# Performance work log

Measured on AMD Instinct MI355X. Metric: run time of the kernel, lower is better.

The kernel has to match this reference:

```python
import jax, jax.numpy as jnp
import numpy as np

B, C, H, W = 2048, 256, 7, 7
EPS = 1e-6  # torch.nn.CosineSimilarity eps


def _masked_cos_loss(f1, f2, A):
    """Fused all-pairs masked cosine similarity.
    f1, f2: [B, C, H, W]; A: [H, W, H, W] binary mask.
    Replaces the original 7x7x7x7 Python loop of per-pixel CosineSimilarity calls.
    Returns per-batch loss [B]: sum_{ijkl: A==1} cos(f1[:,:,i,j], f2[:,:,k,l]) / (H*W*H*W).
    """
    n1 = jnp.linalg.norm(f1, axis=1)  # [B, H, W]
    n2 = jnp.linalg.norm(f2, axis=1)  # [B, H, W]
    dot = jnp.einsum('bcij,bckl->bijkl', f1, f2)  # [B, H, W, H, W]
    denom = jnp.maximum(n1[:, :, :, None, None] * n2[:, None, None, :, :], EPS)
    cos = dot / denom
    mask = (A == 1).astype(f1.dtype)
    return jnp.einsum('bijkl,ijkl->b', cos, mask) / (H * W * H * W)


def setup_inputs() -> dict:
    key = jax.random.key(0)
    k1, k2, k3, k4 = jax.random.split(key, 4)
    base_feature = jax.random.normal(k1, (B, C, H, W), dtype=jnp.float32)
    moment_feature = jax.random.normal(k2, (B, C, H, W), dtype=jnp.float32)
    base_A = jax.random.randint(k3, (H, W, H, W), 0, 2, dtype=jnp.int32)
    moment_A = jax.random.randint(k4, (H, W, H, W), 0, 2, dtype=jnp.int32)
    return {"base_feature": base_feature, "moment_feature": moment_feature,
            "base_A": base_A, "moment_A": moment_A}


def reference(base_feature, moment_feature, base_A, moment_A):
    # base_loss  = masked cos(base[i,j],   moment[k,l]) under base_A
    # moment_loss = masked cos(moment[i,j], base[k,l])  under moment_A
    base_loss = _masked_cos_loss(base_feature, moment_feature, base_A)
    moment_loss = _masked_cos_loss(moment_feature, base_feature, moment_A)
    return -base_loss - moment_loss  # [B]
```

## Files before the change

### kernel.cpp

```cpp
#include <hip/hip_runtime.h>
#include <math.h>


constexpr int NB     = 2048;
constexpr int NC     = 256;
constexpr int NP     = 49;
constexpr int SLAB_C = 16;
constexpr int SLAB_F = SLAB_C * NP;
constexpr int NSLAB  = NC / SLAB_C;
constexpr float EPS  = 1e-6f;

__global__ __launch_bounds__(256, 2)
void pixpro_kernel(const float* __restrict__ gbase,
                   const float* __restrict__ gmom,
                   const int*   __restrict__ A1,
                   const int*   __restrict__ A2,
                   float*       __restrict__ out)
{
    __shared__ float wt[NP * NP];
    __shared__ __align__(16) float slab[4][2 * SLAB_F];

    const int tid  = threadIdx.x;
    const int wave = tid >> 6;
    const int lane = tid & 63;
    const int b    = blockIdx.x * 4 + wave;

    for (int t = tid; t < NP * NP; t += 256) {
        int p = t / NP, q = t - p * NP;
        wt[t] = (A1[t] == 1 ? 1.0f : 0.0f) + (A2[q * NP + p] == 1 ? 1.0f : 0.0f);
    }
    __syncthreads();

    float* sl = slab[wave];

    const int lp = lane & 7, lq = lane >> 3;
    const int p0 = (lp < 7 ? lp : 6) * 7;
    const int q0 = (lq < 7 ? lq : 6) * 7;

    const float* gb = gbase + (size_t)b * (NC * NP);
    const float* gm = gmom  + (size_t)b * (NC * NP);

    const float* vA = sl + ((lane < NP) ? lane : (SLAB_F - NP + lane));
    const float* vB = sl + (SLAB_F + 15 + (lane < 34 ? lane : 33));
    const float* bp = sl + p0;
    const float* mp = sl + SLAB_F + q0;

    float acc[7][7];
    #pragma unroll
    for (int j = 0; j < 7; ++j)
        #pragma unroll
        for (int i = 0; i < 7; ++i) acc[j][i] = 0.0f;
    float nrm0 = 0.0f, nrm1 = 0.0f;

    float4 rb0 = {}, rb1 = {}, rb2 = {}, rb3 = {};
    float4 rm0 = {}, rm1 = {}, rm2 = {}, rm3 = {};
    {
        const float4* pb = (const float4*)gb;
        const float4* pm = (const float4*)gm;
        rb0 = pb[lane]; rb1 = pb[lane + 64]; rb2 = pb[lane + 128];
        rm0 = pm[lane]; rm1 = pm[lane + 64]; rm2 = pm[lane + 128];
        if (lane < 4) { rb3 = pb[lane + 192]; rm3 = pm[lane + 192]; }
    }

    for (int s = 0; s < NSLAB; ++s) {
        {
            float4* lb = (float4*)sl;
            float4* lm = (float4*)(sl + SLAB_F);
            lb[lane] = rb0; lb[lane + 64] = rb1; lb[lane + 128] = rb2;
            lm[lane] = rm0; lm[lane + 64] = rm1; lm[lane + 128] = rm2;
            if (lane < 4) { lb[lane + 192] = rb3; lm[lane + 192] = rm3; }
        }
        if (s + 1 < NSLAB) {
            const float4* pb = (const float4*)(gb + (s + 1) * SLAB_F);
            const float4* pm = (const float4*)(gm + (s + 1) * SLAB_F);
            rb0 = pb[lane]; rb1 = pb[lane + 64]; rb2 = pb[lane + 128];
            rm0 = pm[lane]; rm1 = pm[lane + 64]; rm2 = pm[lane + 128];
            if (lane < 4) { rb3 = pb[lane + 192]; rm3 = pm[lane + 192]; }
        }
        __syncthreads();

        #pragma unroll
        for (int c = 0; c < SLAB_C; ++c) {
            float bv[7], mv[7];
            #pragma unroll
            for (int i = 0; i < 7; ++i) bv[i] = bp[c * NP + i];
            #pragma unroll
            for (int j = 0; j < 7; ++j) mv[j] = mp[c * NP + j];
            float v0 = vA[c * NP];
            float v1 = vB[c * NP];
            nrm0 = fmaf(v0, v0, nrm0);
            nrm1 = fmaf(v1, v1, nrm1);
            #pragma unroll
            for (int j = 0; j < 7; ++j)
                #pragma unroll
                for (int i = 0; i < 7; ++i)
                    acc[j][i] = fmaf(bv[i], mv[j], acc[j][i]);
        }
        __syncthreads();
    }

    float* nsq = sl;
    nsq[lane] = nrm0;
    if (lane < 34) nsq[64 + lane] = nrm1;
    __syncthreads();

    float nbv[7], nmv[7];
    #pragma unroll
    for (int i = 0; i < 7; ++i) nbv[i] = sqrtf(nsq[p0 + i]);
    #pragma unroll
    for (int j = 0; j < 7; ++j) nmv[j] = sqrtf(nsq[NP + q0 + j]);

    float sum = 0.0f;
    if (lp < 7 && lq < 7) {
        #pragma unroll
        for (int j = 0; j < 7; ++j) {
            #pragma unroll
            for (int i = 0; i < 7; ++i) {
                float w     = wt[(p0 + i) * NP + (q0 + j)];
                float denom = fmaxf(nbv[i] * nmv[j], EPS);
                sum += w * acc[j][i] / denom;
            }
        }
    }

    #pragma unroll
    for (int m = 32; m; m >>= 1) sum += __shfl_xor(sum, m, 64);

    if (lane == 0) out[b] = sum * (-1.0f / 2401.0f);
}

extern "C" void kernel_launch(void* const* d_in, const int* in_sizes, int n_in,
                              void* d_out, int out_size, void* d_ws, size_t ws_size,
                              hipStream_t stream)
{
    (void)in_sizes; (void)n_in; (void)d_ws; (void)ws_size; (void)out_size;
    const float* base = (const float*)d_in[0];
    const float* mom  = (const float*)d_in[1];
    const int*   A1   = (const int*)d_in[2];
    const int*   A2   = (const int*)d_in[3];
    float*       out  = (float*)d_out;

    pixpro_kernel<<<NB / 4, 256, 0, stream>>>(base, mom, A1, A2, out);
}
```

Before: 243.5 us.

## Split channel reduction across two waves per batch with transposed LDS layout

Each batch is now handled by two waves, each reducing half of the channels, with partial dot products and norms combined through shared memory at the end. The LDS slab is transposed to a pixel-major layout with pitch 12 so the inner loop can use float4 reads along channels. Block-wide barriers in the main loop become per-wave lgkmcnt waits, the mask table is stored as bytes, and occupancy is raised to 4 blocks per SM. This doubles the number of waves to expose more parallelism and reduce LDS load instructions. The cost is an extra cross-wave reduction of 49 accumulators per thread and scattered scalar LDS stores.

```diff
diff --git a/kernel.cpp b/kernel.cpp
--- a/kernel.cpp
+++ b/kernel.cpp
@@ -5,45 +5,60 @@
 constexpr int NB     = 2048;
 constexpr int NC     = 256;
 constexpr int NP     = 49;
-constexpr int SLAB_C = 16;
-constexpr int SLAB_F = SLAB_C * NP;
-constexpr int NSLAB  = NC / SLAB_C;
+constexpr int SLAB_C = 8;
+constexpr int PITCH  = 12;
+constexpr int FWORDS = NP * PITCH;
+constexpr int REGION = 1280;
+constexpr int NSLABW = (NC / 2) / SLAB_C;
 constexpr float EPS  = 1e-6f;
 
-__global__ __launch_bounds__(256, 2)
+__global__ __launch_bounds__(256, 4)
 void pixpro_kernel(const float* __restrict__ gbase,
                    const float* __restrict__ gmom,
                    const int*   __restrict__ A1,
                    const int*   __restrict__ A2,
                    float*       __restrict__ out)
 {
-    __shared__ float wt[NP * NP];
-    __shared__ __align__(16) float slab[4][2 * SLAB_F];
+    __shared__ unsigned char wtb[NP * NP];
+    __shared__ __align__(16) float slab[4][REGION];
 
     const int tid  = threadIdx.x;
     const int wave = tid >> 6;
     const int lane = tid & 63;
-    const int b    = blockIdx.x * 4 + wave;
+    const int b    = blockIdx.x * 2 + (wave >> 1);
+    const int half = wave & 1;
 
     for (int t = tid; t < NP * NP; t += 256) {
         int p = t / NP, q = t - p * NP;
-        wt[t] = (A1[t] == 1 ? 1.0f : 0.0f) + (A2[q * NP + p] == 1 ? 1.0f : 0.0f);
+        wtb[t] = (unsigned char)((A1[t] == 1 ? 1 : 0) + (A2[q * NP + p] == 1 ? 1 : 0));
     }
     __syncthreads();
 
-    float* sl = slab[wave];
+    float* const sl  = slab[wave];
+    float* const slb = sl;
+    float* const slm = sl + FWORDS;
 
     const int lp = lane & 7, lq = lane >> 3;
     const int p0 = (lp < 7 ? lp : 6) * 7;
     const int q0 = (lq < 7 ? lq : 6) * 7;
 
-    const float* gb = gbase + (size_t)b * (NC * NP);
-    const float* gm = gmom  + (size_t)b * (NC * NP);
+    const float* gb = gbase + (size_t)b * (NC * NP) + (size_t)half * (128 * NP);
+    const float* gm = gmom  + (size_t)b * (NC * NP) + (size_t)half * (128 * NP);
 
-    const float* vA = sl + ((lane < NP) ? lane : (SLAB_F - NP + lane));
-    const float* vB = sl + (SLAB_F + 15 + (lane < 34 ? lane : 33));
-    const float* bp = sl + p0;
-    const float* mp = sl + SLAB_F + q0;
+    int wof[8];
+    #pragma unroll
+    for (int u = 0; u < 4; ++u) {
+        int e  = 4 * lane + u;
+        wof[u] = (e - 49 * (e / 49)) * PITCH + (e / 49);
+        int e2 = (lane < 34) ? (256 + 4 * lane + u) : 391;
+        wof[4 + u] = (e2 - 49 * (e2 / 49)) * PITCH + (e2 / 49);
+    }
+
+    const float* const vA = (lane < NP) ? (slb + lane * PITCH)
+                                        : (slm + (lane - NP) * PITCH);
+    const float* const vB = slm + ((lane < 34) ? (15 + lane) : 48) * PITCH;
+    const float* const bp = slb + p0 * PITCH;
+    const float* const mp = slm + q0 * PITCH;
 
     float acc[7][7];
     #pragma unroll
@@ -52,81 +67,110 @@
         for (int i = 0; i < 7; ++i) acc[j][i] = 0.0f;
     float nrm0 = 0.0f, nrm1 = 0.0f;
 
-    float4 rb0 = {}, rb1 = {}, rb2 = {}, rb3 = {};
-    float4 rm0 = {}, rm1 = {}, rm2 = {}, rm3 = {};
+    float4 rb0 = {}, rb1 = {}, rm0 = {}, rm1 = {};
     {
         const float4* pb = (const float4*)gb;
         const float4* pm = (const float4*)gm;
-        rb0 = pb[lane]; rb1 = pb[lane + 64]; rb2 = pb[lane + 128];
-        rm0 = pm[lane]; rm1 = pm[lane + 64]; rm2 = pm[lane + 128];
-        if (lane < 4) { rb3 = pb[lane + 192]; rm3 = pm[lane + 192]; }
+        rb0 = pb[lane]; rm0 = pm[lane];
+        if (lane < 34) { rb1 = pb[64 + lane]; rm1 = pm[64 + lane]; }
     }
 
-    for (int s = 0; s < NSLAB; ++s) {
-        {
-            float4* lb = (float4*)sl;
-            float4* lm = (float4*)(sl + SLAB_F);
-            lb[lane] = rb0; lb[lane + 64] = rb1; lb[lane + 128] = rb2;
-            lm[lane] = rm0; lm[lane + 64] = rm1; lm[lane + 128] = rm2;
-            if (lane < 4) { lb[lane + 192] = rb3; lm[lane + 192] = rm3; }
+    for (int s = 0; s < NSLABW; ++s) {
+        slb[wof[0]] = rb0.x; slb[wof[1]] = rb0.y; slb[wof[2]] = rb0.z; slb[wof[3]] = rb0.w;
+        slm[wof[0]] = rm0.x; slm[wof[1]] = rm0.y; slm[wof[2]] = rm0.z; slm[wof[3]] = rm0.w;
+        if (lane < 34) {
+            slb[wof[4]] = rb1.x; slb[wof[5]] = rb1.y; slb[wof[6]] = rb1.z; slb[wof[7]] = rb1.w;
+            slm[wof[4]] = rm1.x; slm[wof[5]] = rm1.y; slm[wof[6]] = rm1.z; slm[wof[7]] = rm1.w;
         }
-        if (s + 1 < NSLAB) {
-            const float4* pb = (const float4*)(gb + (s + 1) * SLAB_F);
-            const float4* pm = (const float4*)(gm + (s + 1) * SLAB_F);
-            rb0 = pb[lane]; rb1 = pb[lane + 64]; rb2 = pb[lane + 128];
-            rm0 = pm[lane]; rm1 = pm[lane + 64]; rm2 = pm[lane + 128];
-            if (lane < 4) { rb3 = pb[lane + 192]; rm3 = pm[lane + 192]; }
+        if (s + 1 < NSLABW) {
+            const float4* pb = (const float4*)(gb + (s + 1) * (SLAB_C * NP));
+            const float4* pm = (const float4*)(gm + (s + 1) * (SLAB_C * NP));
+            rb0 = pb[lane]; rm0 = pm[lane];
+            if (lane < 34) { rb1 = pb[64 + lane]; rm1 = pm[64 + lane]; }
         }
-        __syncthreads();
+        asm volatile("s_waitcnt lgkmcnt(0)" ::: "memory");
 
         #pragma unroll
-        for (int c = 0; c < SLAB_C; ++c) {
-            float bv[7], mv[7];
+        for (int c0 = 0; c0 < SLAB_C; c0 += 4) {
+            float4 mv[7];
             #pragma unroll
-            for (int i = 0; i < 7; ++i) bv[i] = bp[c * NP + i];
+            for (int j = 0; j < 7; ++j)
+                mv[j] = *(const float4*)(mp + j * PITCH + c0);
+            float4 a4 = *(const float4*)(vA + c0);
+            float4 b4 = *(const float4*)(vB + c0);
+            nrm0 = fmaf(a4.x, a4.x, fmaf(a4.y, a4.y, fmaf(a4.z, a4.z, fmaf(a4.w, a4.w, nrm0))));
+            nrm1 = fmaf(b4.x, b4.x, fmaf(b4.y, b4.y, fmaf(b4.z, b4.z, fmaf(b4.w, b4.w, nrm1))));
             #pragma unroll
-            for (int j = 0; j < 7; ++j) mv[j] = mp[c * NP + j];
-            float v0 = vA[c * NP];
-            float v1 = vB[c * NP];
-            nrm0 = fmaf(v0, v0, nrm0);
-            nrm1 = fmaf(v1, v1, nrm1);
+            for (int i = 0; i < 7; ++i) {
+                float4 bv = *(const float4*)(bp + i * PITCH + c0);
+                #pragma unroll
+                for (int j = 0; j < 7; ++j) {
+                    float t0 = fmaf(bv.x, mv[j].x, acc[j][i]);
+                    t0       = fmaf(bv.y, mv[j].y, t0);
+                    t0       = fmaf(bv.z, mv[j].z, t0);
+                    acc[j][i] = fmaf(bv.w, mv[j].w, t0);
+                }
+            }
+        }
+        asm volatile("s_waitcnt lgkmcnt(0)" ::: "memory");
+    }
+
+    __syncthreads();
+
+    float* const ex   = slab[wave & ~1];
+    const bool active = (lp < 7) && (lq < 7);
+    const int  tix    = lq * 7 + lp;
+
+    if (half) {
+        ex[lane]      = nrm0;
+        ex[64 + lane] = nrm1;
+        if (active) {
             #pragma unroll
             for (int j = 0; j < 7; ++j)
                 #pragma unroll
                 for (int i = 0; i < 7; ++i)
-                    acc[j][i] = fmaf(bv[i], mv[j], acc[j][i]);
+                    ex[128 + tix * 49 + j * 7 + i] = acc[j][i];
         }
-        __syncthreads();
     }
-
-    float* nsq = sl;
-    nsq[lane] = nrm0;
-    if (lane < 34) nsq[64 + lane] = nrm1;
     __syncthreads();
 
-    float nbv[7], nmv[7];
-    #pragma unroll
-    for (int i = 0; i < 7; ++i) nbv[i] = sqrtf(nsq[p0 + i]);
-    #pragma unroll
-    for (int j = 0; j < 7; ++j) nmv[j] = sqrtf(nsq[NP + q0 + j]);
+    if (!half) {
+        nrm0 += ex[lane];
+        nrm1 += ex[64 + lane];
+        if (active) {
+            #pragma unroll
+            for (int j = 0; j < 7; ++j)
+                #pragma unroll
+                for (int i = 0; i < 7; ++i)
+                    acc[j][i] += ex[128 + tix * 49 + j * 7 + i];
+        }
+        asm volatile("s_waitcnt lgkmcnt(0)" ::: "memory");
 
-    float sum = 0.0f;
-    if (lp < 7 && lq < 7) {
+        ex[lane] = nrm0;
+        if (lane < 34) ex[64 + lane] = nrm1;
+        asm volatile("s_waitcnt lgkmcnt(0)" ::: "memory");
+
+        float nbv[7], nmv[7];
         #pragma unroll
-        for (int j = 0; j < 7; ++j) {
+        for (int i = 0; i < 7; ++i) nbv[i] = sqrtf(ex[p0 + i]);
+        #pragma unroll
+        for (int j = 0; j < 7; ++j) nmv[j] = sqrtf(ex[NP + q0 + j]);
+
+        float sum = 0.0f;
+        if (active) {
             #pragma unroll
-            for (int i = 0; i < 7; ++i) {
-                float w     = wt[(p0 + i) * NP + (q0 + j)];
-                float denom = fmaxf(nbv[i] * nmv[j], EPS);
-                sum += w * acc[j][i] / denom;
-            }
+            for (int j = 0; j < 7; ++j)
+                #pragma unroll
+                for (int i = 0; i < 7; ++i) {
+                    float w     = (float)wtb[(p0 + i) * NP + (q0 + j)];
+                    float denom = fmaxf(nbv[i] * nmv[j], EPS);
+                    sum += w * acc[j][i] / denom;
+                }
         }
+        #pragma unroll
+        for (int m = 32; m; m >>= 1) sum += __shfl_xor(sum, m, 64);
+        if (lane == 0) out[b] = sum * (-1.0f / 2401.0f);
     }
-
-    #pragma unroll
-    for (int m = 32; m; m >>= 1) sum += __shfl_xor(sum, m, 64);
-
-    if (lane == 0) out[b] = sum * (-1.0f / 2401.0f);
 }
 
 extern "C" void kernel_launch(void* const* d_in, const int* in_sizes, int n_in,
@@ -140,5 +184,5 @@
     const int*   A2   = (const int*)d_in[3];
     float*       out  = (float*)d_out;
 
-    pixpro_kernel<<<NB / 4, 256, 0, stream>>>(base, mom, A1, A2, out);
+    pixpro_kernel<<<NB / 2, 256, 0, stream>>>(base, mom, A1, A2, out);
 }
```

Result: slower. 479.4 us (+96.8%).

## Use split-bf16 MFMA for the pixel Gram matrix, one batch per block

Applied to the files above, without the earlier changes.

Replaces the per-lane scalar FMA 49x49 dot-product accumulation with bf16 MFMA 16x16x32 instructions. Each fp32 input is split into hi and lo bf16 parts and three products are summed, approximating fp32 accuracy. The work is reorganized so one 256-thread block handles a single batch, with four waves each taking a 16-row strip. Panels of 32 channels are double-buffered in LDS with register prefetch. The aim is to move the compute-bound GEMM onto matrix cores, at the cost of conversion overhead, padding of 49 up to 64, and a small accuracy loss from dropping the lo*lo term.

```diff
diff --git a/kernel.cpp b/kernel.cpp
--- a/kernel.cpp
+++ b/kernel.cpp
@@ -2,13 +2,18 @@
 #include <math.h>
 
 
-constexpr int NB     = 2048;
-constexpr int NC     = 256;
-constexpr int NP     = 49;
-constexpr int SLAB_C = 16;
-constexpr int SLAB_F = SLAB_C * NP;
-constexpr int NSLAB  = NC / SLAB_C;
-constexpr float EPS  = 1e-6f;
+constexpr int NB  = 2048;
+constexpr int NC  = 256;
+constexpr int NP  = 49;
+constexpr float EPS = 1e-6f;
+
+constexpr int PW      = 40;
+constexpr int MROW    = 49;
+constexpr int BUFROWS = 4 * MROW;
+constexpr int TOTROWS = 2 * BUFROWS + 15;
+
+typedef short bf16x8 __attribute__((ext_vector_type(8)));
+typedef float f32x4  __attribute__((ext_vector_type(4)));
 
 __global__ __launch_bounds__(256, 2)
 void pixpro_kernel(const float* __restrict__ gbase,
@@ -17,116 +22,141 @@
                    const int*   __restrict__ A2,
                    float*       __restrict__ out)
 {
-    __shared__ float wt[NP * NP];
-    __shared__ __align__(16) float slab[4][2 * SLAB_F];
+    __shared__ unsigned char wtb[NP * NP];
+    __shared__ __align__(16) unsigned short mats[TOTROWS * PW];
+    __shared__ float nbp[4][NP], nmp[4][NP];
+    __shared__ float sbc[NP], smc[NP];
+    __shared__ float redsum[4];
 
     const int tid  = threadIdx.x;
     const int wave = tid >> 6;
     const int lane = tid & 63;
-    const int b    = blockIdx.x * 4 + wave;
+    const int b    = blockIdx.x;
 
     for (int t = tid; t < NP * NP; t += 256) {
         int p = t / NP, q = t - p * NP;
-        wt[t] = (A1[t] == 1 ? 1.0f : 0.0f) + (A2[q * NP + p] == 1 ? 1.0f : 0.0f);
+        wtb[t] = (unsigned char)((A1[t] == 1 ? 1 : 0) + (A2[q * NP + p] == 1 ? 1 : 0));
+    }
+
+    const float* gB = gbase + (size_t)b * (NC * NP);
+    const float* gM = gmom  + (size_t)b * (NC * NP);
+    const bool   ld = (lane < NP);
+
+    float nrmb = 0.f, nrmm = 0.f;
+
+    auto LOADS = [&](int panel, float (&x)[2][8]) {
+        if (!ld) return;
+        const float* pB = gB + (32 * panel + 8 * wave) * NP + lane;
+        const float* pM = gM + (32 * panel + 8 * wave) * NP + lane;
+        #pragma unroll
+        for (int j = 0; j < 8; ++j) x[0][j] = pB[j * NP];
+        #pragma unroll
+        for (int j = 0; j < 8; ++j) x[1][j] = pM[j * NP];
+    };
+
+    auto CVTWRITE = [&](int buf, float (&x)[2][8]) {
+        if (!ld) return;
+        #pragma unroll
+        for (int f = 0; f < 2; ++f) {
+            unsigned int hi[4], lo[4];
+            float n = 0.f;
+            #pragma unroll
+            for (int jp = 0; jp < 4; ++jp) {
+                float x0 = x[f][2 * jp], x1 = x[f][2 * jp + 1];
+                unsigned int u0 = __float_as_uint(x0) & 0xFFFF0000u;
+                unsigned int u1 = __float_as_uint(x1) & 0xFFFF0000u;
+                hi[jp] = u1 | (u0 >> 16);
+                float l0 = x0 - __uint_as_float(u0);
+                float l1 = x1 - __uint_as_float(u1);
+                unsigned int r;
+                asm("v_cvt_pk_bf16_f32 %0, %1, %2" : "=v"(r) : "v"(l0), "v"(l1));
+                lo[jp] = r;
+                n = fmaf(x0, x0, fmaf(x1, x1, n));
+            }
+            if (f == 0) nrmb += n; else nrmm += n;
+            unsigned short* mh = mats + ((size_t)buf * BUFROWS + (2 * f + 0) * MROW + lane) * PW + 8 * wave;
+            unsigned short* ml = mats + ((size_t)buf * BUFROWS + (2 * f + 1) * MROW + lane) * PW + 8 * wave;
+            *reinterpret_cast<uint4*>(mh) = make_uint4(hi[0], hi[1], hi[2], hi[3]);
+            *reinterpret_cast<uint4*>(ml) = make_uint4(lo[0], lo[1], lo[2], lo[3]);
+        }
+    };
+
+    f32x4 acc[4];
+    const f32x4 zz = {0.f, 0.f, 0.f, 0.f};
+    acc[0] = zz; acc[1] = zz; acc[2] = zz; acc[3] = zz;
+
+    const int fr = lane & 15;
+    const int kc = lane >> 4;
+
+    auto COMPUTE = [&](int buf) {
+        const unsigned short* mb = mats + (size_t)buf * BUFROWS * PW;
+        const unsigned short* pA = mb + (16 * wave + fr) * PW + kc * 8;
+        bf16x8 Ah = *(const bf16x8*)(pA);
+        bf16x8 Al = *(const bf16x8*)(pA + MROW * PW);
+        #pragma unroll
+        for (int t = 0; t < 4; ++t) {
+            const unsigned short* pBm = mb + (2 * MROW + 16 * t + fr) * PW + kc * 8;
+            bf16x8 Bh = *(const bf16x8*)(pBm);
+            bf16x8 Bl = *(const bf16x8*)(pBm + MROW * PW);
+            acc[t] = __builtin_amdgcn_mfma_f32_16x16x32_bf16(Ah, Bh, acc[t], 0, 0, 0);
+            acc[t] = __builtin_amdgcn_mfma_f32_16x16x32_bf16(Ah, Bl, acc[t], 0, 0, 0);
+            acc[t] = __builtin_amdgcn_mfma_f32_16x16x32_bf16(Al, Bh, acc[t], 0, 0, 0);
+        }
+    };
+
+    {
+        float x0[2][8];
+        LOADS(0, x0);
+        CVTWRITE(0, x0);
     }
     __syncthreads();
 
-    float* sl = slab[wave];
-
-    const int lp = lane & 7, lq = lane >> 3;
-    const int p0 = (lp < 7 ? lp : 6) * 7;
-    const int q0 = (lq < 7 ? lq : 6) * 7;
-
-    const float* gb = gbase + (size_t)b * (NC * NP);
-    const float* gm = gmom  + (size_t)b * (NC * NP);
-
-    const float* vA = sl + ((lane < NP) ? lane : (SLAB_F - NP + lane));
-    const float* vB = sl + (SLAB_F + 15 + (lane < 34 ? lane : 33));
-    const float* bp = sl + p0;
-    const float* mp = sl + SLAB_F + q0;
-
-    float acc[7][7];
-    #pragma unroll
-    for (int j = 0; j < 7; ++j)
-        #pragma unroll
-        for (int i = 0; i < 7; ++i) acc[j][i] = 0.0f;
-    float nrm0 = 0.0f, nrm1 = 0.0f;
-
-    float4 rb0 = {}, rb1 = {}, rb2 = {}, rb3 = {};
-    float4 rm0 = {}, rm1 = {}, rm2 = {}, rm3 = {};
-    {
-        const float4* pb = (const float4*)gb;
-        const float4* pm = (const float4*)gm;
-        rb0 = pb[lane]; rb1 = pb[lane + 64]; rb2 = pb[lane + 128];
-        rm0 = pm[lane]; rm1 = pm[lane + 64]; rm2 = pm[lane + 128];
-        if (lane < 4) { rb3 = pb[lane + 192]; rm3 = pm[lane + 192]; }
-    }
-
-    for (int s = 0; s < NSLAB; ++s) {
-        {
-            float4* lb = (float4*)sl;
-            float4* lm = (float4*)(sl + SLAB_F);
-            lb[lane] = rb0; lb[lane + 64] = rb1; lb[lane + 128] = rb2;
-            lm[lane] = rm0; lm[lane + 64] = rm1; lm[lane + 128] = rm2;
-            if (lane < 4) { lb[lane + 192] = rb3; lm[lane + 192] = rm3; }
-        }
-        if (s + 1 < NSLAB) {
-            const float4* pb = (const float4*)(gb + (s + 1) * SLAB_F);
-            const float4* pm = (const float4*)(gm + (s + 1) * SLAB_F);
-            rb0 = pb[lane]; rb1 = pb[lane + 64]; rb2 = pb[lane + 128];
-            rm0 = pm[lane]; rm1 = pm[lane + 64]; rm2 = pm[lane + 128];
-            if (lane < 4) { rb3 = pb[lane + 192]; rm3 = pm[lane + 192]; }
-        }
-        __syncthreads();
-
-        #pragma unroll
-        for (int c = 0; c < SLAB_C; ++c) {
-            float bv[7], mv[7];
-            #pragma unroll
-            for (int i = 0; i < 7; ++i) bv[i] = bp[c * NP + i];
-            #pragma unroll
-            for (int j = 0; j < 7; ++j) mv[j] = mp[c * NP + j];
-            float v0 = vA[c * NP];
-            float v1 = vB[c * NP];
-            nrm0 = fmaf(v0, v0, nrm0);
-            nrm1 = fmaf(v1, v1, nrm1);
-            #pragma unroll
-            for (int j = 0; j < 7; ++j)
-                #pragma unroll
-                for (int i = 0; i < 7; ++i)
-                    acc[j][i] = fmaf(bv[i], mv[j], acc[j][i]);
-        }
+    #pragma unroll 2
+    for (int k = 0; k < 8; ++k) {
+        float xn[2][8];
+        if (k + 1 < 8) LOADS(k + 1, xn);
+        COMPUTE(k & 1);
+        if (k + 1 < 8) CVTWRITE((k & 1) ^ 1, xn);
         __syncthreads();
     }
 
-    float* nsq = sl;
-    nsq[lane] = nrm0;
-    if (lane < 34) nsq[64 + lane] = nrm1;
+    if (ld) { nbp[wave][lane] = nrmb; nmp[wave][lane] = nrmm; }
+    __syncthreads();
+    if (wave == 0 && ld) {
+        sbc[lane] = nbp[0][lane] + nbp[1][lane] + nbp[2][lane] + nbp[3][lane];
+        smc[lane] = nmp[0][lane] + nmp[1][lane] + nmp[2][lane] + nmp[3][lane];
+    }
     __syncthreads();
 
-    float nbv[7], nmv[7];
+    float nbr[4];
     #pragma unroll
-    for (int i = 0; i < 7; ++i) nbv[i] = sqrtf(nsq[p0 + i]);
+    for (int r = 0; r < 4; ++r) {
+        int row = 16 * wave + 4 * kc + r;
+        nbr[r] = (row < NP) ? sqrtf(sbc[row]) : 0.f;
+    }
+    float sum = 0.f;
     #pragma unroll
-    for (int j = 0; j < 7; ++j) nmv[j] = sqrtf(nsq[NP + q0 + j]);
-
-    float sum = 0.0f;
-    if (lp < 7 && lq < 7) {
-        #pragma unroll
-        for (int j = 0; j < 7; ++j) {
+    for (int t = 0; t < 4; ++t) {
+        int col = 16 * t + fr;
+        if (col < NP) {
+            float nmc = sqrtf(smc[col]);
             #pragma unroll
-            for (int i = 0; i < 7; ++i) {
-                float w     = wt[(p0 + i) * NP + (q0 + j)];
-                float denom = fmaxf(nbv[i] * nmv[j], EPS);
-                sum += w * acc[j][i] / denom;
+            for (int r = 0; r < 4; ++r) {
+                int row = 16 * wave + 4 * kc + r;
+                if (row < NP) {
+                    float w     = (float)wtb[row * NP + col];
+                    float denom = fmaxf(nbr[r] * nmc, EPS);
+                    sum += w * acc[t][r] / denom;
+                }
             }
         }
     }
-
     #pragma unroll
     for (int m = 32; m; m >>= 1) sum += __shfl_xor(sum, m, 64);
-
-    if (lane == 0) out[b] = sum * (-1.0f / 2401.0f);
+    if (lane == 0) redsum[wave] = sum;
+    __syncthreads();
+    if (tid == 0)
+        out[b] = -(redsum[0] + redsum[1] + redsum[2] + redsum[3]) * (1.0f / 2401.0f);
 }
 
 extern "C" void kernel_launch(void* const* d_in, const int* in_sizes, int n_in,
@@ -140,5 +170,5 @@
     const int*   A2   = (const int*)d_in[3];
     float*       out  = (float*)d_out;
 
-    pixpro_kernel<<<NB / 4, 256, 0, stream>>>(base, mom, A1, A2, out);
+    pixpro_kernel<<<NB, 256, 0, stream>>>(base, mom, A1, A2, out);
 }
```

After: 229.2 us. 1.06x faster.
